# Optimization experiments

Hardware: AMD Instinct MI355X
Metric: run time of the kernel (lower is better)

The kernel has to match this reference:

```python
import jax, jax.numpy as jnp
import numpy as np

B, S, D = 64, 512, 768
H1, H2, NC = 256, 128, 1
THR = 0.1  # attention_threshold in original forward


def setup_inputs() -> dict:
    key = jax.random.key(0)
    k0, k1, k2, k3 = jax.random.split(key, 4)
    # scale hidden states so H @ H^T logits are in a reasonable softmax range
    hidden_states = jax.random.normal(k0, (B, S, D), jnp.float32) * 0.05
    attention_mask = jnp.ones((B, S), jnp.int32)
    W1 = jax.random.normal(k1, (D, H1), jnp.float32) * (1.0 / np.sqrt(D))
    b1 = jnp.zeros((H1,), jnp.float32)
    W2 = jax.random.normal(k2, (H1, H2), jnp.float32) * (1.0 / np.sqrt(H1))
    b2 = jnp.zeros((H2,), jnp.float32)
    Wc = jax.random.normal(k3, (H2, NC), jnp.float32) * (1.0 / np.sqrt(H2))
    bc = jnp.zeros((NC,), jnp.float32)
    return dict(hidden_states=hidden_states, attention_mask=attention_mask,
                W1=W1, b1=b1, W2=W2, b2=b2, Wc=Wc, bc=bc)


def _gcn_adj(att):
    # thresholded sparse graph, expressed as masked dense adjacency [B,S,S]
    A = jnp.where(att > THR, att, 0.0)
    # PyG add_remaining_self_loops: keep existing self-loop weight, else fill 1.0
    diag = jnp.diagonal(att, axis1=-2, axis2=-1)            # [B,S]
    diag = jnp.where(diag > THR, diag, 1.0)
    i = jnp.arange(att.shape[-1])
    A = A.at[:, i, i].set(diag)
    # gcn_norm: deg over targets (columns), D^{-1/2} A D^{-1/2}
    deg = A.sum(axis=-2)                                     # [B,S]
    dis = jnp.where(deg > 0, jax.lax.rsqrt(deg), 0.0)
    return dis[:, :, None] * A * dis[:, None, :]


def _gcn_layer(Ahat, x, W, b):
    xw = x @ W                                               # linear first (no bias)
    # out[target j] = sum_source i  Ahat[i,j] * xw[i]
    return jnp.einsum('bij,bih->bjh', Ahat, xw) + b


def reference(hidden_states, attention_mask, W1, b1, W2, b2, Wc, bc):
    att = jax.nn.softmax(
        jnp.einsum('bsd,btd->bst', hidden_states, hidden_states), axis=-1)
    Ahat = _gcn_adj(att)                                     # [B,S,S]
    x = jax.nn.relu(_gcn_layer(Ahat, hidden_states, W1, b1))  # dropout inactive (eval)
    x = _gcn_layer(Ahat, x, W2, b2)                          # [B,S,H2]
    m = attention_mask.astype(x.dtype)                       # masked mean over valid tokens
    emb = (x * m[:, :, None]).sum(axis=1) / m.sum(axis=1, keepdims=True)
    return jax.nn.sigmoid(emb @ Wc + bc)                     # [B,1]
```

## Files before the change

### kernel.cpp

```cpp
#include <hip/hip_runtime.h>
#include <hip/hip_bf16.h>
#include <math.h>

constexpr int B = 64, S = 512, D = 768, H1 = 256, H2 = 128;
constexpr float THR = 0.1f;

typedef short bf16x8 __attribute__((ext_vector_type(8)));
typedef float f32x4 __attribute__((ext_vector_type(4)));
typedef unsigned int uint_t;
typedef const __attribute__((address_space(1))) unsigned int* gptr_t;
typedef __attribute__((address_space(3))) unsigned int* lptr_t;

__device__ __forceinline__ unsigned short f2bf(float f) {
    unsigned int u = __builtin_bit_cast(unsigned int, f);
    unsigned int r = (u + 0x7FFFu + ((u >> 16) & 1u)) >> 16;
    return (unsigned short)r;
}
__device__ __forceinline__ float bf2f(unsigned short b) {
    return __builtin_bit_cast(float, (unsigned int)b << 16);
}
__device__ __forceinline__ void unpack8(const uint4& r, float* v) {
    v[0] = __builtin_bit_cast(float, r.x << 16); v[1] = __builtin_bit_cast(float, r.x & 0xFFFF0000u);
    v[2] = __builtin_bit_cast(float, r.y << 16); v[3] = __builtin_bit_cast(float, r.y & 0xFFFF0000u);
    v[4] = __builtin_bit_cast(float, r.z << 16); v[5] = __builtin_bit_cast(float, r.z & 0xFFFF0000u);
    v[6] = __builtin_bit_cast(float, r.w << 16); v[7] = __builtin_bit_cast(float, r.w & 0xFFFF0000u);
}
__device__ __forceinline__ void gl2lds16(const void* g, void* l) {
    __builtin_amdgcn_global_load_lds((gptr_t)g, (lptr_t)l, 16, 0, 0);
}

__global__ __launch_bounds__(256) void k_cast(const float* __restrict__ in,
                                              short* __restrict__ out,
                                              const float* __restrict__ W1,
                                              short* __restrict__ W1T,
                                              const float* __restrict__ W2,
                                              short* __restrict__ W2T,
                                              float* __restrict__ zbuf) {
    const int id = blockIdx.x * 256 + threadIdx.x;
    if (id < 18432) ((float4*)zbuf)[id] = make_float4(0.f, 0.f, 0.f, 0.f);
    if (id < 196608) {
        const int n = id / D, k = id - n * D;
        W1T[id] = (short)f2bf(W1[(size_t)k * H1 + n]);
    } else if (id < 229376) {
        const int i2 = id - 196608;
        const int n = i2 / H1, k = i2 - n * H1;
        W2T[i2] = (short)f2bf(W2[(size_t)k * H2 + n]);
    }
    for (int i = id; i < 3145728; i += 524288) {
        float4 a = ((const float4*)in)[i * 2];
        float4 b = ((const float4*)in)[i * 2 + 1];
        uint4 o;
        o.x = (uint_t)f2bf(a.x) | ((uint_t)f2bf(a.y) << 16);
        o.y = (uint_t)f2bf(a.z) | ((uint_t)f2bf(a.w) << 16);
        o.z = (uint_t)f2bf(b.x) | ((uint_t)f2bf(b.y) << 16);
        o.w = (uint_t)f2bf(b.z) | ((uint_t)f2bf(b.w) << 16);
        ((uint4*)out)[i] = o;
    }
}

__global__ __launch_bounds__(256) void k_logits(const short* __restrict__ Hb_,
                                                short* __restrict__ L,
                                                float* __restrict__ rsum) {
    const int orig = blockIdx.x;
    const int wg = (orig & 7) * 128 + (orig >> 3);
    const int bz = wg >> 4;
    const int bi = (wg >> 2) & 3, bj = wg & 3;
    const short* Ab = Hb_ + (size_t)bz * S * D;
    short* Lb = L + (size_t)bz * S * S;
    float* rs = rsum + bz * S;
    const int M0 = bi * 128, N0 = bj * 128;

    __shared__ __align__(16) short As[8192];
    __shared__ __align__(16) short Bs[8192];

    const int tid = threadIdx.x, lane = tid & 63, wid = tid >> 6;
    const int wm = (wid & 1) * 64, wn = (wid >> 1) * 64;
    const int r_in = lane >> 3, kc = lane & 7;
    const int kswz = ((kc ^ r_in) << 3);

    f32x4 zero = {0.f, 0.f, 0.f, 0.f};
    f32x4 acc[4][4];
    #pragma unroll
    for (int mi = 0; mi < 4; ++mi)
        #pragma unroll
        for (int nj = 0; nj < 4; ++nj) acc[mi][nj] = zero;

    for (int t = 0; t < 12; ++t) {
        const int kt = t * 64;
        #pragma unroll
        for (int q = 0; q < 4; ++q) {
            const int ch = wid * 4 + q;
            gl2lds16(Ab + (size_t)(M0 + ch * 8 + r_in) * D + kt + kswz, &As[ch * 512]);
        }
        #pragma unroll
        for (int q = 0; q < 4; ++q) {
            const int ch = wid * 4 + q;
            gl2lds16(Ab + (size_t)(N0 + ch * 8 + r_in) * D + kt + kswz, &Bs[ch * 512]);
        }
        __syncthreads();
        #pragma unroll
        for (int kk = 0; kk < 2; ++kk) {
            bf16x8 af[4], bfr[4];
            const int g0 = kk * 4 + (lane >> 4);
            #pragma unroll
            for (int mi = 0; mi < 4; ++mi) {
                const int row = wm + mi * 16 + (lane & 15);
                af[mi] = *(const bf16x8*)&As[row * 64 + ((g0 ^ (row & 7)) << 3)];
            }
            #pragma unroll
            for (int nj = 0; nj < 4; ++nj) {
                const int row = wn + nj * 16 + (lane & 15);
                bfr[nj] = *(const bf16x8*)&Bs[row * 64 + ((g0 ^ (row & 7)) << 3)];
            }
            #pragma unroll
            for (int mi = 0; mi < 4; ++mi)
                #pragma unroll
                for (int nj = 0; nj < 4; ++nj)
                    acc[mi][nj] = __builtin_amdgcn_mfma_f32_16x16x32_bf16(
                        af[mi], bfr[nj], acc[mi][nj], 0, 0, 0);
        }
        __syncthreads();
    }

    #pragma unroll
    for (int mi = 0; mi < 4; ++mi)
        #pragma unroll
        for (int nj = 0; nj < 4; ++nj) {
            f32x4 v = acc[mi][nj];
            acc[mi][nj][0] = __expf(v[0]);
            acc[mi][nj][1] = __expf(v[1]);
            acc[mi][nj][2] = __expf(v[2]);
            acc[mi][nj][3] = __expf(v[3]);
        }

    #pragma unroll
    for (int mi = 0; mi < 4; ++mi) {
        const int mb = wm + mi * 16 + (lane >> 4) * 4;
        #pragma unroll
        for (int nj = 0; nj < 4; ++nj) {
            const int n = wn + nj * 16 + (lane & 15);
            f32x4 v = acc[mi][nj];
            ushort4 o = make_ushort4(f2bf(v[0]), f2bf(v[1]), f2bf(v[2]), f2bf(v[3]));
            *(ushort4*)&Lb[(size_t)(N0 + n) * S + M0 + mb] = o;
        }
    }

    #pragma unroll
    for (int mi = 0; mi < 4; ++mi)
        #pragma unroll
        for (int r = 0; r < 4; ++r) {
            float s = acc[mi][0][r] + acc[mi][1][r] + acc[mi][2][r] + acc[mi][3][r];
            s += __shfl_xor(s, 1); s += __shfl_xor(s, 2);
            s += __shfl_xor(s, 4); s += __shfl_xor(s, 8);
            if ((lane & 15) == 0)
                atomicAdd(&rs[M0 + wm + mi * 16 + (lane >> 4) * 4 + r], s);
        }
}

__global__ __launch_bounds__(256) void k_prep(const short* __restrict__ L,
                                              const float* __restrict__ rsum,
                                              const int* __restrict__ mask,
                                              float* __restrict__ dis,
                                              float* __restrict__ wacc,
                                              uint_t* __restrict__ ents,
                                              uint_t* __restrict__ cnts) {
    const int j = blockIdx.x * 4 + (threadIdx.x >> 6);
    const int lane = threadIdx.x & 63;
    const int b = j >> 9, jl = j & (S - 1);
    const size_t base = (size_t)b * S * S + (size_t)jl * S + lane * 8;
    uint4 r = *(const uint4*)(L + base);
    float v[8];
    unpack8(r, v);
    const int i0 = lane * 8;
    const float4 sa = *(const float4*)&rsum[b * S + i0];
    const float4 sb = *(const float4*)&rsum[b * S + i0 + 4];
    const float rsv[8] = {sa.x, sa.y, sa.z, sa.w, sb.x, sb.y, sb.z, sb.w};
    float a[8];
    float deg = 0.f;
    #pragma unroll
    for (int e = 0; e < 8; ++e) {
        float att = v[e] / rsv[e];
        if (i0 + e == jl) a[e] = (att > THR) ? att : 1.0f;
        else              a[e] = (att > THR) ? att : 0.0f;
        deg += a[e];
    }
    #pragma unroll
    for (int off = 1; off < 64; off <<= 1) deg += __shfl_xor(deg, off);
    const float d = (deg > 0.f) ? rsqrtf(deg) : 0.f;
    const float cv = d * (float)mask[j];
    if (lane == 0) dis[j] = d;
    #pragma unroll
    for (int e = 0; e < 8; ++e)
        if (a[e] != 0.f) atomicAdd(&wacc[b * S + i0 + e], cv * a[e]);

    unsigned long long bl[8];
    #pragma unroll
    for (int e = 0; e < 8; ++e) bl[e] = __ballot(a[e] != 0.f);
    const unsigned long long lt = (lane == 0) ? 0ull : (~0ull >> (64 - lane));
    int pre = 0, tot = 0;
    #pragma unroll
    for (int e = 0; e < 8; ++e) {
        pre += __popcll(bl[e] & lt);
        tot += __popcll(bl[e]);
    }
    uint_t* rowents = ents + (size_t)j * S;
    int own = 0;
    #pragma unroll
    for (int e = 0; e < 8; ++e) {
        if (a[e] != 0.f) {
            rowents[pre + own] = ((uint_t)(i0 + e) << 16) | (uint_t)f2bf(a[e]);
            ++own;
        }
    }
    if (lane == 0) cnts[j] = (uint_t)tot;
}

__global__ __launch_bounds__(256) void k_agg(const uint_t* __restrict__ ents,
                                             const uint_t* __restrict__ cnts,
                                             const float* __restrict__ dis,
                                             const short* __restrict__ xw1d,
                                             const float* __restrict__ b1,
                                             short* __restrict__ y1) {
    const int j = blockIdx.x;
    const int b = j >> 9;
    const int tid = threadIdx.x;
    const int cnt = (int)cnts[j];
    __shared__ uint_t sents[S];
    for (int k = tid; k < cnt; k += 256) sents[k] = ents[(size_t)j * S + k];
    __syncthreads();
    const int h = tid;
    float acc = 0.f;
    for (int k = 0; k < cnt; ++k) {
        const uint_t p = sents[k];
        const int i = (int)(p >> 16);
        const float val = bf2f((unsigned short)(p & 0xFFFFu));
        acc += val * bf2f((unsigned short)xw1d[(size_t)(b * S + i) * H1 + h]);
    }
    const float o = fmaxf(dis[j] * acc + b1[h], 0.f);
    y1[(size_t)j * H1 + h] = (short)f2bf(o);
}

template <int MODE, int TN, int GX>
__global__ __launch_bounds__(256) void k_gemm(
    const short* __restrict__ A, const short* __restrict__ Bm, short* __restrict__ C,
    int K, int lda, int ldb, int ldc,
    const float* __restrict__ sN, const float* __restrict__ sN2,
    float* __restrict__ embp) {
    constexpr int NJ = TN / 32;
    const int nwg = gridDim.x;
    const int orig = blockIdx.x;
    const int wg = (orig & 7) * (nwg >> 3) + (orig >> 3);
    const int bx = wg % GX, by = wg / GX;
    const int M0 = bx * 128, N0 = by * TN;

    __shared__ __align__(16) short As[128 * 64];
    __shared__ __align__(16) short Bs[TN * 64];

    const int tid = threadIdx.x, lane = tid & 63, wid = tid >> 6;
    const int wm = (wid & 1) * 64, wn = (wid >> 1) * (TN / 2);
    const int r_in = lane >> 3, kc = lane & 7;
    const int kswz = ((kc ^ r_in) << 3);

    f32x4 zero = {0.f, 0.f, 0.f, 0.f};
    f32x4 acc[4][NJ];
    #pragma unroll
    for (int mi = 0; mi < 4; ++mi)
        #pragma unroll
        for (int nj = 0; nj < NJ; ++nj) acc[mi][nj] = zero;

    const int nt = K >> 6;
    for (int t = 0; t < nt; ++t) {
        const int kt = t << 6;
        #pragma unroll
        for (int q = 0; q < 4; ++q) {
            const int ch = wid * 4 + q;
            gl2lds16(A + (size_t)(M0 + ch * 8 + r_in) * lda + kt + kswz, &As[ch * 512]);
        }
        #pragma unroll
        for (int q = 0; q < NJ; ++q) {
            const int ch = wid * NJ + q;
            gl2lds16(Bm + (size_t)(N0 + ch * 8 + r_in) * ldb + kt + kswz, &Bs[ch * 512]);
        }
        __syncthreads();
        #pragma unroll
        for (int kk = 0; kk < 2; ++kk) {
            bf16x8 af[4], bfr[NJ];
            const int g0 = kk * 4 + (lane >> 4);
            #pragma unroll
            for (int mi = 0; mi < 4; ++mi) {
                const int row = wm + mi * 16 + (lane & 15);
                af[mi] = *(const bf16x8*)&As[row * 64 + ((g0 ^ (row & 7)) << 3)];
            }
            #pragma unroll
            for (int nj = 0; nj < NJ; ++nj) {
                const int row = wn + nj * 16 + (lane & 15);
                bfr[nj] = *(const bf16x8*)&Bs[row * 64 + ((g0 ^ (row & 7)) << 3)];
            }
            #pragma unroll
            for (int mi = 0; mi < 4; ++mi)
                #pragma unroll
                for (int nj = 0; nj < NJ; ++nj)
                    acc[mi][nj] = __builtin_amdgcn_mfma_f32_16x16x32_bf16(
                        af[mi], bfr[nj], acc[mi][nj], 0, 0, 0);
        }
        __syncthreads();
    }

    if (MODE == 3) {
        #pragma unroll
        for (int mi = 0; mi < 4; ++mi) {
            const int m = M0 + wm + mi * 16 + (lane >> 4) * 4;
            #pragma unroll
            for (int nj = 0; nj < NJ; ++nj) {
                const int n = N0 + wn + nj * 16 + (lane & 15);
                f32x4 v = acc[mi][nj];
                const float sn = sN[n];
                ushort4 o = make_ushort4(f2bf(v[0] * sn), f2bf(v[1] * sn),
                                         f2bf(v[2] * sn), f2bf(v[3] * sn));
                *(ushort4*)&C[(size_t)n * ldc + m] = o;
            }
        }
    } else {
        const int bb = N0 >> 9;
        float wv[NJ];
        #pragma unroll
        for (int nj = 0; nj < NJ; ++nj) {
            const int gn = N0 + wn + nj * 16 + (lane & 15);
            wv[nj] = sN[gn] * sN2[gn];
        }
        #pragma unroll
        for (int mi = 0; mi < 4; ++mi)
            #pragma unroll
            for (int r = 0; r < 4; ++r) {
                float s = 0.f;
                #pragma unroll
                for (int nj = 0; nj < NJ; ++nj) s += acc[mi][nj][r] * wv[nj];
                s += __shfl_xor(s, 1); s += __shfl_xor(s, 2);
                s += __shfl_xor(s, 4); s += __shfl_xor(s, 8);
                if ((lane & 15) == 0) {
                    const int h = M0 + wm + mi * 16 + (lane >> 4) * 4 + r;
                    atomicAdd(&embp[bb * H2 + h], s);
                }
            }
    }
}

__global__ __launch_bounds__(128) void k_final(const float* __restrict__ emb,
                                               const int* __restrict__ mask,
                                               const float* __restrict__ b2,
                                               const float* __restrict__ Wc,
                                               const float* __restrict__ bc,
                                               float* __restrict__ out) {
    const int b = blockIdx.x;
    const int h = threadIdx.x;
    const int* mb = mask + b * S;

    float msum = 0.f;
    for (int i = h; i < S; i += 128) msum += (float)mb[i];
    #pragma unroll
    for (int off = 1; off < 64; off <<= 1) msum += __shfl_xor(msum, off);
    __shared__ float redm[2], redv[2];
    if ((h & 63) == 0) redm[h >> 6] = msum;
    __syncthreads();
    msum = redm[0] + redm[1];

    const float e = b2[h] + emb[b * H2 + h] / msum;
    float val = e * Wc[h];
    #pragma unroll
    for (int off = 1; off < 64; off <<= 1) val += __shfl_xor(val, off);
    if ((h & 63) == 0) redv[h >> 6] = val;
    __syncthreads();
    if (h == 0) {
        float z = redv[0] + redv[1] + bc[0];
        out[b] = 1.f / (1.f + expf(-z));
    }
}

extern "C" void kernel_launch(void* const* d_in, const int* in_sizes, int n_in,
                              void* d_out, int out_size, void* d_ws, size_t ws_size,
                              hipStream_t stream) {
    const float* H    = (const float*)d_in[0];
    const int*   mask = (const int*)d_in[1];
    const float* W1   = (const float*)d_in[2];
    const float* b1   = (const float*)d_in[3];
    const float* W2   = (const float*)d_in[4];
    const float* b2   = (const float*)d_in[5];
    const float* Wc   = (const float*)d_in[6];
    const float* bc   = (const float*)d_in[7];
    float* out = (float*)d_out;

    const int NTOK = B * S;

    char* wsb = (char*)d_ws;
    short* Hb    = (short*)(wsb);
    short* y1    = (short*)(wsb);
    short* Lbuf  = (short*)(wsb + 50331648);
    short* xw1d  = (short*)(wsb + 83886080);
    float* rsum  = (float*)(wsb + 109051904);
    float* wacc  = rsum + NTOK;
    float* emb   = wacc + NTOK;
    float* dis   = emb + 8192;
    short* W1T   = (short*)(dis + NTOK);
    short* W2T   = W1T + 196608;
    uint_t* ents = (uint_t*)(wsb + 134217728);
    uint_t* cnts = (uint_t*)(wsb + 201326592);

    k_cast<<<2048, 256, 0, stream>>>(H, Hb, W1, W1T, W2, W2T, rsum);

    k_logits<<<1024, 256, 0, stream>>>(Hb, Lbuf, rsum);

    k_prep<<<NTOK / 4, 256, 0, stream>>>(Lbuf, rsum, mask, dis, wacc, ents, cnts);

    k_gemm<3, 64, 2><<<1024, 256, 0, stream>>>(
        W1T, Hb, xw1d, D, D, D, H1, dis, nullptr, nullptr);

    k_agg<<<NTOK, 256, 0, stream>>>(ents, cnts, dis, xw1d, b1, y1);

    k_gemm<4, 64, 1><<<512, 256, 0, stream>>>(
        W2T, y1, nullptr, H1, H1, H1, 0, wacc, dis, emb);

    k_final<<<B, 128, 0, stream>>>(emb, mask, b2, Wc, bc, out);
}
```

Baseline: 148.8 us.

## Store exp logits as fp8, fuse prep with XW1 GEMM, batch aggregation rows

Exponentiated logits are stored as a custom 8-bit float (4-bit exponent, 3-bit mantissa) instead of bf16, halving the adjacency buffer's write and read traffic. The prep pass and the first linear GEMM are merged into one launch, interleaving 8 prep blocks with 1 GEMM block so the two independent jobs overlap. Because the GEMM no longer scales by dis, the aggregation kernel now applies the source-node dis itself and handles 8 rows per block. The coarser fp8 quantization of attention values near the 0.1 threshold may change which edges survive and could hurt accuracy.

```diff
diff --git a/kernel.cpp b/kernel.cpp
--- a/kernel.cpp
+++ b/kernel.cpp
@@ -19,11 +19,15 @@
 __device__ __forceinline__ float bf2f(unsigned short b) {
     return __builtin_bit_cast(float, (unsigned int)b << 16);
 }
-__device__ __forceinline__ void unpack8(const uint4& r, float* v) {
-    v[0] = __builtin_bit_cast(float, r.x << 16); v[1] = __builtin_bit_cast(float, r.x & 0xFFFF0000u);
-    v[2] = __builtin_bit_cast(float, r.y << 16); v[3] = __builtin_bit_cast(float, r.y & 0xFFFF0000u);
-    v[4] = __builtin_bit_cast(float, r.z << 16); v[5] = __builtin_bit_cast(float, r.z & 0xFFFF0000u);
-    v[6] = __builtin_bit_cast(float, r.w << 16); v[7] = __builtin_bit_cast(float, r.w & 0xFFFF0000u);
+__device__ __forceinline__ unsigned char f2fp8(float f) {
+    uint_t u = __builtin_bit_cast(uint_t, f);
+    u += 0x7FFFFu + ((u >> 20) & 1u);
+    return (unsigned char)((((u >> 23) - 120u) << 3) | ((u >> 20) & 7u));
+}
+__device__ __forceinline__ float fp82f(unsigned char q) {
+    uint_t e = (q >> 3) & 0xFu, m = q & 7u;
+    if (e == 0) return (float)m * 0.001953125f;
+    return __builtin_bit_cast(float, ((e + 120u) << 23) | (m << 20));
 }
 __device__ __forceinline__ void gl2lds16(const void* g, void* l) {
     __builtin_amdgcn_global_load_lds((gptr_t)g, (lptr_t)l, 16, 0, 0);
@@ -59,14 +63,14 @@
 }
 
 __global__ __launch_bounds__(256) void k_logits(const short* __restrict__ Hb_,
-                                                short* __restrict__ L,
+                                                unsigned char* __restrict__ L8,
                                                 float* __restrict__ rsum) {
     const int orig = blockIdx.x;
     const int wg = (orig & 7) * 128 + (orig >> 3);
     const int bz = wg >> 4;
     const int bi = (wg >> 2) & 3, bj = wg & 3;
     const short* Ab = Hb_ + (size_t)bz * S * D;
-    short* Lb = L + (size_t)bz * S * S;
+    unsigned char* Lb = L8 + (size_t)bz * S * S;
     float* rs = rsum + bz * S;
     const int M0 = bi * 128, N0 = bj * 128;
 
@@ -140,8 +144,10 @@
         for (int nj = 0; nj < 4; ++nj) {
             const int n = wn + nj * 16 + (lane & 15);
             f32x4 v = acc[mi][nj];
-            ushort4 o = make_ushort4(f2bf(v[0]), f2bf(v[1]), f2bf(v[2]), f2bf(v[3]));
-            *(ushort4*)&Lb[(size_t)(N0 + n) * S + M0 + mb] = o;
+            uchar4 o;
+            o.x = f2fp8(v[0]); o.y = f2fp8(v[1]);
+            o.z = f2fp8(v[2]); o.w = f2fp8(v[3]);
+            *(uchar4*)&Lb[(size_t)(N0 + n) * S + M0 + mb] = o;
         }
     }
 
@@ -157,134 +163,206 @@
         }
 }
 
-__global__ __launch_bounds__(256) void k_prep(const short* __restrict__ L,
-                                              const float* __restrict__ rsum,
-                                              const int* __restrict__ mask,
-                                              float* __restrict__ dis,
-                                              float* __restrict__ wacc,
-                                              uint_t* __restrict__ ents,
-                                              uint_t* __restrict__ cnts) {
-    const int j = blockIdx.x * 4 + (threadIdx.x >> 6);
-    const int lane = threadIdx.x & 63;
-    const int b = j >> 9, jl = j & (S - 1);
-    const size_t base = (size_t)b * S * S + (size_t)jl * S + lane * 8;
-    uint4 r = *(const uint4*)(L + base);
-    float v[8];
-    unpack8(r, v);
-    const int i0 = lane * 8;
-    const float4 sa = *(const float4*)&rsum[b * S + i0];
-    const float4 sb = *(const float4*)&rsum[b * S + i0 + 4];
-    const float rsv[8] = {sa.x, sa.y, sa.z, sa.w, sb.x, sb.y, sb.z, sb.w};
-    float a[8];
-    float deg = 0.f;
-    #pragma unroll
-    for (int e = 0; e < 8; ++e) {
-        float att = v[e] / rsv[e];
-        if (i0 + e == jl) a[e] = (att > THR) ? att : 1.0f;
-        else              a[e] = (att > THR) ? att : 0.0f;
-        deg += a[e];
-    }
-    #pragma unroll
-    for (int off = 1; off < 64; off <<= 1) deg += __shfl_xor(deg, off);
-    const float d = (deg > 0.f) ? rsqrtf(deg) : 0.f;
-    const float cv = d * (float)mask[j];
-    if (lane == 0) dis[j] = d;
-    #pragma unroll
-    for (int e = 0; e < 8; ++e)
-        if (a[e] != 0.f) atomicAdd(&wacc[b * S + i0 + e], cv * a[e]);
-
-    unsigned long long bl[8];
-    #pragma unroll
-    for (int e = 0; e < 8; ++e) bl[e] = __ballot(a[e] != 0.f);
-    const unsigned long long lt = (lane == 0) ? 0ull : (~0ull >> (64 - lane));
-    int pre = 0, tot = 0;
-    #pragma unroll
-    for (int e = 0; e < 8; ++e) {
-        pre += __popcll(bl[e] & lt);
-        tot += __popcll(bl[e]);
-    }
-    uint_t* rowents = ents + (size_t)j * S;
-    int own = 0;
-    #pragma unroll
-    for (int e = 0; e < 8; ++e) {
-        if (a[e] != 0.f) {
-            rowents[pre + own] = ((uint_t)(i0 + e) << 16) | (uint_t)f2bf(a[e]);
-            ++own;
-        }
-    }
-    if (lane == 0) cnts[j] = (uint_t)tot;
+__global__ __launch_bounds__(256) void k_prep_gemm(
+    const unsigned char* __restrict__ L8, const float* __restrict__ rsum,
+    const int* __restrict__ mask, float* __restrict__ dis,
+    float* __restrict__ wacc, uint_t* __restrict__ ents, uint_t* __restrict__ cnts,
+    const short* __restrict__ W1T, const short* __restrict__ Hb,
+    short* __restrict__ xw1) {
+    __shared__ __align__(16) short As[128 * 64];
+    __shared__ __align__(16) short Bs[64 * 64];
+
+    const int blk = blockIdx.x;
+    const int r9 = blk % 9;
+    const int tid = threadIdx.x, lane = tid & 63, wid = tid >> 6;
+
+    if (r9 != 8) {
+        const int p = (blk / 9) * 8 + r9;
+        const int j = p * 4 + (tid >> 6);
+        const int b = j >> 9, jl = j & (S - 1);
+        const size_t base = (size_t)b * S * S + (size_t)jl * S + lane * 8;
+        const uint2 r = *(const uint2*)(L8 + base);
+        const int i0 = lane * 8;
+        const float4 sa = *(const float4*)&rsum[b * S + i0];
+        const float4 sb = *(const float4*)&rsum[b * S + i0 + 4];
+        const float rsv[8] = {sa.x, sa.y, sa.z, sa.w, sb.x, sb.y, sb.z, sb.w};
+        float a[8];
+        float deg = 0.f;
+        #pragma unroll
+        for (int e = 0; e < 8; ++e) {
+            const unsigned char q = (e < 4) ? (unsigned char)(r.x >> (e * 8))
+                                            : (unsigned char)(r.y >> ((e - 4) * 8));
+            float att = fp82f(q) / rsv[e];
+            if (i0 + e == jl) a[e] = (att > THR) ? att : 1.0f;
+            else              a[e] = (att > THR) ? att : 0.0f;
+            deg += a[e];
+        }
+        #pragma unroll
+        for (int off = 1; off < 64; off <<= 1) deg += __shfl_xor(deg, off);
+        const float d = (deg > 0.f) ? rsqrtf(deg) : 0.f;
+        const float cv = d * (float)mask[j];
+        if (lane == 0) dis[j] = d;
+        #pragma unroll
+        for (int e = 0; e < 8; ++e)
+            if (a[e] != 0.f) atomicAdd(&wacc[b * S + i0 + e], cv * a[e]);
+
+        unsigned long long bl[8];
+        #pragma unroll
+        for (int e = 0; e < 8; ++e) bl[e] = __ballot(a[e] != 0.f);
+        const unsigned long long lt = (lane == 0) ? 0ull : (~0ull >> (64 - lane));
+        int pre = 0, tot = 0;
+        #pragma unroll
+        for (int e = 0; e < 8; ++e) {
+            pre += __popcll(bl[e] & lt);
+            tot += __popcll(bl[e]);
+        }
+        uint_t* rowents = ents + (size_t)j * S;
+        int own = 0;
+        #pragma unroll
+        for (int e = 0; e < 8; ++e) {
+            if (a[e] != 0.f) {
+                rowents[pre + own] = ((uint_t)(i0 + e) << 16) | (uint_t)f2bf(a[e]);
+                ++own;
+            }
+        }
+        if (lane == 0) cnts[j] = (uint_t)tot;
+        return;
+    }
+
+    const int orig = blk / 9;
+    const int wg = (orig & 7) * 128 + (orig >> 3);
+    const int bx = wg & 1, by = wg >> 1;
+    const int M0 = bx * 128, N0 = by * 64;
+
+    const int wm = (wid & 1) * 64, wn = (wid >> 1) * 32;
+    const int r_in = lane >> 3, kc = lane & 7;
+    const int kswz = ((kc ^ r_in) << 3);
+
+    f32x4 zero = {0.f, 0.f, 0.f, 0.f};
+    f32x4 acc[4][2];
+    #pragma unroll
+    for (int mi = 0; mi < 4; ++mi) {
+        acc[mi][0] = zero; acc[mi][1] = zero;
+    }
+
+    for (int t = 0; t < 12; ++t) {
+        const int kt = t << 6;
+        #pragma unroll
+        for (int q = 0; q < 4; ++q) {
+            const int ch = wid * 4 + q;
+            gl2lds16(W1T + (size_t)(M0 + ch * 8 + r_in) * D + kt + kswz, &As[ch * 512]);
+        }
+        #pragma unroll
+        for (int q = 0; q < 2; ++q) {
+            const int ch = wid * 2 + q;
+            gl2lds16(Hb + (size_t)(N0 + ch * 8 + r_in) * D + kt + kswz, &Bs[ch * 512]);
+        }
+        __syncthreads();
+        #pragma unroll
+        for (int kk = 0; kk < 2; ++kk) {
+            bf16x8 af[4], bfr[2];
+            const int g0 = kk * 4 + (lane >> 4);
+            #pragma unroll
+            for (int mi = 0; mi < 4; ++mi) {
+                const int row = wm + mi * 16 + (lane & 15);
+                af[mi] = *(const bf16x8*)&As[row * 64 + ((g0 ^ (row & 7)) << 3)];
+            }
+            #pragma unroll
+            for (int nj = 0; nj < 2; ++nj) {
+                const int row = wn + nj * 16 + (lane & 15);
+                bfr[nj] = *(const bf16x8*)&Bs[row * 64 + ((g0 ^ (row & 7)) << 3)];
+            }
+            #pragma unroll
+            for (int mi = 0; mi < 4; ++mi)
+                #pragma unroll
+                for (int nj = 0; nj < 2; ++nj)
+                    acc[mi][nj] = __builtin_amdgcn_mfma_f32_16x16x32_bf16(
+                        af[mi], bfr[nj], acc[mi][nj], 0, 0, 0);
+        }
+        __syncthreads();
+    }
+
+    #pragma unroll
+    for (int mi = 0; mi < 4; ++mi) {
+        const int m = M0 + wm + mi * 16 + (lane >> 4) * 4;
+        #pragma unroll
+        for (int nj = 0; nj < 2; ++nj) {
+            const int n = N0 + wn + nj * 16 + (lane & 15);
+            f32x4 v = acc[mi][nj];
+            ushort4 o = make_ushort4(f2bf(v[0]), f2bf(v[1]), f2bf(v[2]), f2bf(v[3]));
+            *(ushort4*)&xw1[(size_t)n * H1 + m] = o;
+        }
+    }
 }
 
 __global__ __launch_bounds__(256) void k_agg(const uint_t* __restrict__ ents,
                                              const uint_t* __restrict__ cnts,
                                              const float* __restrict__ dis,
-                                             const short* __restrict__ xw1d,
+                                             const short* __restrict__ xw1,
                                              const float* __restrict__ b1,
                                              short* __restrict__ y1) {
-    const int j = blockIdx.x;
-    const int b = j >> 9;
     const int tid = threadIdx.x;
-    const int cnt = (int)cnts[j];
+    const int h = tid;
+    const float bias = b1[h];
     __shared__ uint_t sents[S];
-    for (int k = tid; k < cnt; k += 256) sents[k] = ents[(size_t)j * S + k];
-    __syncthreads();
-    const int h = tid;
-    float acc = 0.f;
-    for (int k = 0; k < cnt; ++k) {
-        const uint_t p = sents[k];
-        const int i = (int)(p >> 16);
-        const float val = bf2f((unsigned short)(p & 0xFFFFu));
-        acc += val * bf2f((unsigned short)xw1d[(size_t)(b * S + i) * H1 + h]);
-    }
-    const float o = fmaxf(dis[j] * acc + b1[h], 0.f);
-    y1[(size_t)j * H1 + h] = (short)f2bf(o);
-}
-
-template <int MODE, int TN, int GX>
-__global__ __launch_bounds__(256) void k_gemm(
-    const short* __restrict__ A, const short* __restrict__ Bm, short* __restrict__ C,
-    int K, int lda, int ldb, int ldc,
-    const float* __restrict__ sN, const float* __restrict__ sN2,
+    for (int jj = 0; jj < 8; ++jj) {
+        const int j = blockIdx.x * 8 + jj;
+        const int b = j >> 9;
+        const int cnt = (int)cnts[j];
+        for (int k = tid; k < cnt; k += 256) sents[k] = ents[(size_t)j * S + k];
+        __syncthreads();
+        float acc = 0.f;
+        for (int k = 0; k < cnt; ++k) {
+            const uint_t p = sents[k];
+            const int i = (int)(p >> 16);
+            const float val = bf2f((unsigned short)(p & 0xFFFFu)) * dis[b * S + i];
+            acc += val * bf2f((unsigned short)xw1[(size_t)(b * S + i) * H1 + h]);
+        }
+        const float o = fmaxf(dis[j] * acc + bias, 0.f);
+        y1[(size_t)j * H1 + h] = (short)f2bf(o);
+        __syncthreads();
+    }
+}
+
+__global__ __launch_bounds__(256) void k_gemm_emb(
+    const short* __restrict__ W2T, const short* __restrict__ y1,
+    const float* __restrict__ wacc, const float* __restrict__ dis,
     float* __restrict__ embp) {
-    constexpr int NJ = TN / 32;
-    const int nwg = gridDim.x;
     const int orig = blockIdx.x;
-    const int wg = (orig & 7) * (nwg >> 3) + (orig >> 3);
-    const int bx = wg % GX, by = wg / GX;
-    const int M0 = bx * 128, N0 = by * TN;
+    const int wg = (orig & 7) * 64 + (orig >> 3);
+    const int N0 = wg * 64;
 
     __shared__ __align__(16) short As[128 * 64];
-    __shared__ __align__(16) short Bs[TN * 64];
+    __shared__ __align__(16) short Bs[64 * 64];
 
     const int tid = threadIdx.x, lane = tid & 63, wid = tid >> 6;
-    const int wm = (wid & 1) * 64, wn = (wid >> 1) * (TN / 2);
+    const int wm = (wid & 1) * 64, wn = (wid >> 1) * 32;
     const int r_in = lane >> 3, kc = lane & 7;
     const int kswz = ((kc ^ r_in) << 3);
 
     f32x4 zero = {0.f, 0.f, 0.f, 0.f};
-    f32x4 acc[4][NJ];
-    #pragma unroll
-    for (int mi = 0; mi < 4; ++mi)
-        #pragma unroll
-        for (int nj = 0; nj < NJ; ++nj) acc[mi][nj] = zero;
-
-    const int nt = K >> 6;
-    for (int t = 0; t < nt; ++t) {
+    f32x4 acc[4][2];
+    #pragma unroll
+    for (int mi = 0; mi < 4; ++mi) {
+        acc[mi][0] = zero; acc[mi][1] = zero;
+    }
+
+    for (int t = 0; t < 4; ++t) {
         const int kt = t << 6;
         #pragma unroll
         for (int q = 0; q < 4; ++q) {
             const int ch = wid * 4 + q;
-            gl2lds16(A + (size_t)(M0 + ch * 8 + r_in) * lda + kt + kswz, &As[ch * 512]);
-        }
-        #pragma unroll
-        for (int q = 0; q < NJ; ++q) {
-            const int ch = wid * NJ + q;
-            gl2lds16(Bm + (size_t)(N0 + ch * 8 + r_in) * ldb + kt + kswz, &Bs[ch * 512]);
+            gl2lds16(W2T + (size_t)(ch * 8 + r_in) * H1 + kt + kswz, &As[ch * 512]);
+        }
+        #pragma unroll
+        for (int q = 0; q < 2; ++q) {
+            const int ch = wid * 2 + q;
+            gl2lds16(y1 + (size_t)(N0 + ch * 8 + r_in) * H1 + kt + kswz, &Bs[ch * 512]);
         }
         __syncthreads();
         #pragma unroll
         for (int kk = 0; kk < 2; ++kk) {
-            bf16x8 af[4], bfr[NJ];
+            bf16x8 af[4], bfr[2];
             const int g0 = kk * 4 + (lane >> 4);
             #pragma unroll
             for (int mi = 0; mi < 4; ++mi) {
@@ -292,57 +370,39 @@
                 af[mi] = *(const bf16x8*)&As[row * 64 + ((g0 ^ (row & 7)) << 3)];
             }
             #pragma unroll
-            for (int nj = 0; nj < NJ; ++nj) {
+            for (int nj = 0; nj < 2; ++nj) {
                 const int row = wn + nj * 16 + (lane & 15);
                 bfr[nj] = *(const bf16x8*)&Bs[row * 64 + ((g0 ^ (row & 7)) << 3)];
             }
             #pragma unroll
             for (int mi = 0; mi < 4; ++mi)
                 #pragma unroll
-                for (int nj = 0; nj < NJ; ++nj)
+                for (int nj = 0; nj < 2; ++nj)
                     acc[mi][nj] = __builtin_amdgcn_mfma_f32_16x16x32_bf16(
                         af[mi], bfr[nj], acc[mi][nj], 0, 0, 0);
         }
         __syncthreads();
     }
 
-    if (MODE == 3) {
-        #pragma unroll
-        for (int mi = 0; mi < 4; ++mi) {
-            const int m = M0 + wm + mi * 16 + (lane >> 4) * 4;
-            #pragma unroll
-            for (int nj = 0; nj < NJ; ++nj) {
-                const int n = N0 + wn + nj * 16 + (lane & 15);
-                f32x4 v = acc[mi][nj];
-                const float sn = sN[n];
-                ushort4 o = make_ushort4(f2bf(v[0] * sn), f2bf(v[1] * sn),
-                                         f2bf(v[2] * sn), f2bf(v[3] * sn));
-                *(ushort4*)&C[(size_t)n * ldc + m] = o;
-            }
-        }
-    } else {
-        const int bb = N0 >> 9;
-        float wv[NJ];
-        #pragma unroll
-        for (int nj = 0; nj < NJ; ++nj) {
-            const int gn = N0 + wn + nj * 16 + (lane & 15);
-            wv[nj] = sN[gn] * sN2[gn];
-        }
-        #pragma unroll
-        for (int mi = 0; mi < 4; ++mi)
-            #pragma unroll
-            for (int r = 0; r < 4; ++r) {
-                float s = 0.f;
-                #pragma unroll
-                for (int nj = 0; nj < NJ; ++nj) s += acc[mi][nj][r] * wv[nj];
-                s += __shfl_xor(s, 1); s += __shfl_xor(s, 2);
-                s += __shfl_xor(s, 4); s += __shfl_xor(s, 8);
-                if ((lane & 15) == 0) {
-                    const int h = M0 + wm + mi * 16 + (lane >> 4) * 4 + r;
-                    atomicAdd(&embp[bb * H2 + h], s);
-                }
-            }
-    }
+    const int bb = N0 >> 9;
+    float wv[2];
+    #pragma unroll
+    for (int nj = 0; nj < 2; ++nj) {
+        const int gn = N0 + wn + nj * 16 + (lane & 15);
+        wv[nj] = wacc[gn] * dis[gn];
+    }
+    #pragma unroll
+    for (int mi = 0; mi < 4; ++mi)
+        #pragma unroll
+        for (int r = 0; r < 4; ++r) {
+            float s = acc[mi][0][r] * wv[0] + acc[mi][1][r] * wv[1];
+            s += __shfl_xor(s, 1); s += __shfl_xor(s, 2);
+            s += __shfl_xor(s, 4); s += __shfl_xor(s, 8);
+            if ((lane & 15) == 0) {
+                const int h = wm + mi * 16 + (lane >> 4) * 4 + r;
+                atomicAdd(&embp[bb * H2 + h], s);
+            }
+        }
 }
 
 __global__ __launch_bounds__(128) void k_final(const float* __restrict__ emb,
@@ -394,8 +454,8 @@
     char* wsb = (char*)d_ws;
     short* Hb    = (short*)(wsb);
     short* y1    = (short*)(wsb);
-    short* Lbuf  = (short*)(wsb + 50331648);
-    short* xw1d  = (short*)(wsb + 83886080);
+    unsigned char* Lbuf = (unsigned char*)(wsb + 50331648);
+    short* xw1   = (short*)(wsb + 83886080);
     float* rsum  = (float*)(wsb + 109051904);
     float* wacc  = rsum + NTOK;
     float* emb   = wacc + NTOK;
@@ -409,15 +469,12 @@
 
     k_logits<<<1024, 256, 0, stream>>>(Hb, Lbuf, rsum);
 
-    k_prep<<<NTOK / 4, 256, 0, stream>>>(Lbuf, rsum, mask, dis, wacc, ents, cnts);
-
-    k_gemm<3, 64, 2><<<1024, 256, 0, stream>>>(
-        W1T, Hb, xw1d, D, D, D, H1, dis, nullptr, nullptr);
-
-    k_agg<<<NTOK, 256, 0, stream>>>(ents, cnts, dis, xw1d, b1, y1);
-
-    k_gemm<4, 64, 1><<<512, 256, 0, stream>>>(
-        W2T, y1, nullptr, H1, H1, H1, 0, wacc, dis, emb);
+    k_prep_gemm<<<9216, 256, 0, stream>>>(Lbuf, rsum, mask, dis, wacc, ents, cnts,
+                                          W1T, Hb, xw1);
+
+    k_agg<<<4096, 256, 0, stream>>>(ents, cnts, dis, xw1, b1, y1);
+
+    k_gemm_emb<<<512, 256, 0, stream>>>(W2T, y1, wacc, dis, emb);
 
     k_final<<<B, 128, 0, stream>>>(emb, mask, b2, Wc, bc, out);
 }
```

Result: faster. 142.7 us (-4.1%).
